# Performance work log

Hardware: AMD Instinct MI355X
Metric: run time of the kernel (lower is better)

The kernel has to match this reference:

```python
import jax, jax.numpy as jnp
import numpy as np

VOCAB, D, H, B, S = 50257, 256, 512, 4096, 256
N_NODES, N_WORLDS = 10, 4
# static in-edge lists derived from SEFIROT_PATHS (to_sefirah == i)
IN_EDGES = [[], [0], [0, 1], [1], [2, 3], [2, 4], [1, 3, 5], [4, 5], [5, 6, 7], [6, 7, 8]]

def _gelu(v):
    return jax.nn.gelu(v, approximate=False)

def setup_inputs() -> dict:
    key = jax.random.key(0)
    ks = jax.random.split(key, 24)
    s = 0.02
    inp = {
        "x": jax.random.randint(ks[0], (B, S), 0, VOCAB, dtype=jnp.int64) if jax.config.jax_enable_x64 else jax.random.randint(ks[0], (B, S), 0, VOCAB, dtype=jnp.int32),
        "num_iterations": 3,
        "embed_table": jax.random.normal(ks[1], (VOCAB, D), jnp.float32) * s,
        # per-node processor MLP (stacked over 10 nodes), weights in [in,out] layout
        "node_w1": jax.random.normal(ks[2], (N_NODES, D, D), jnp.float32) * s,
        "node_b1": jnp.zeros((N_NODES, D), jnp.float32),
        "node_w2": jax.random.normal(ks[3], (N_NODES, D, D), jnp.float32) * s,
        "node_b2": jnp.zeros((N_NODES, D), jnp.float32),
        "recv_w": jax.random.normal(ks[4], (N_NODES, D, D), jnp.float32) * s,
        "recv_b": jnp.zeros((N_NODES, D), jnp.float32),
        # four worlds processors
        "world_w1": jax.random.normal(ks[5], (N_WORLDS, D, D), jnp.float32) * s,
        "world_b1": jnp.zeros((N_WORLDS, D), jnp.float32),
        "world_w2": jax.random.normal(ks[6], (N_WORLDS, D, D), jnp.float32) * s,
        "world_b2": jnp.zeros((N_WORLDS, D), jnp.float32),
        # tzimtzum
        "tz_w1": jax.random.normal(ks[7], (D, D // 2), jnp.float32) * s,
        "tz_b1": jnp.zeros((D // 2,), jnp.float32),
        "tz_w2": jax.random.normal(ks[8], (D // 2, D), jnp.float32) * s,
        "tz_b2": jnp.zeros((D,), jnp.float32),
        "void_space": jax.random.normal(ks[9], (D,), jnp.float32) * 0.1,
        "cre_w": jax.random.normal(ks[10], (D, D), jnp.float32) * s,
        "cre_b": jnp.zeros((D,), jnp.float32),
        # shekhinah head
        "shek_w1": jax.random.normal(ks[11], (D, H), jnp.float32) * s,
        "shek_b1": jnp.zeros((H,), jnp.float32),
        "shek_w2": jax.random.normal(ks[12], (H, 1), jnp.float32) * s,
        "shek_b2": jnp.zeros((1,), jnp.float32),
    }
    return inp

def _forward(embed_table, node_w1, node_b1, node_w2, node_b2, recv_w, recv_b,
             world_w1, world_b1, world_w2, world_b2,
             tz_w1, tz_b1, tz_w2, tz_b2, void_space, cre_w, cre_b,
             shek_w1, shek_b1, shek_w2, shek_b2, x, num_iterations):
    # memory-bound embedding gather [B,S,D] + mean over seq -> [B,D]
    embedded = jnp.take(embed_table, x, axis=0).mean(axis=1)
    states = [embedded] * N_NODES
    # sequential light-flow: node i within an iteration sees updated states of j < i
    for _ in range(int(num_iterations)):
        for i in range(N_NODES):
            h = _gelu(states[i] @ node_w1[i] + node_b1[i]) @ node_w2[i] + node_b2[i]
            srcs = IN_EDGES[i]
            if srcs:
                inc = states[srcs[0]]
                for s_ in srcs[1:]:
                    inc = inc + states[s_]
                h = h + inc @ recv_w[i] + recv_b[i]
            states[i] = h
    malkuth = states[9]
    cur = malkuth
    for w in range(N_WORLDS):
        cur = _gelu(cur @ world_w1[w] + world_b1[w]) @ world_w2[w] + world_b2[w]
    contracted = _gelu(cur @ tz_w1 + tz_b1) @ tz_w2 + tz_b2
    created = (contracted + void_space[None, :]) @ cre_w + cre_b
    shek = jax.nn.sigmoid(_gelu(created @ shek_w1 + shek_b1) @ shek_w2 + shek_b2)  # [B,1]
    # pack all outputs: [B, 10*D + D + D + 1]
    stacked = jnp.concatenate(states, axis=-1)
    return jnp.concatenate([stacked, cur, created, shek], axis=-1)

def reference(x, num_iterations, embed_table, node_w1, node_b1, node_w2, node_b2,
              recv_w, recv_b, world_w1, world_b1, world_w2, world_b2,
              tz_w1, tz_b1, tz_w2, tz_b2, void_space, cre_w, cre_b,
              shek_w1, shek_b1, shek_w2, shek_b2):
    return _forward(embed_table, node_w1, node_b1, node_w2, node_b2, recv_w, recv_b,
                    world_w1, world_b1, world_w2, world_b2,
                    tz_w1, tz_b1, tz_w2, tz_b2, void_space, cre_w, cre_b,
                    shek_w1, shek_b1, shek_w2, shek_b2, x, num_iterations)
```

## Files before the change

kernel.cpp:

```cpp
#include <hip/hip_runtime.h>
#include <hip/hip_bf16.h>

#define DIM 256
#define SEQ 256
#define NB 4096
#define OUT_STRIDE 3073

typedef float f32x4 __attribute__((ext_vector_type(4)));
typedef __bf16 bf16x8 __attribute__((ext_vector_type(8)));
typedef unsigned short u16;
typedef unsigned int u32;

__device__ __forceinline__ float bf2f(u16 h){ return __uint_as_float(((u32)h)<<16); }
__device__ __forceinline__ u16 f2bf(float f){
  u32 u = __float_as_uint(f);
  return (u16)((u + 0x7FFFu + ((u>>16)&1u)) >> 16);
}
__device__ __forceinline__ float gelu_f(float x){
  float u = 0.7978845608028654f*(x + 0.044715f*x*x*x);
  float e = __expf(2.0f*u);
  float t = 1.0f - 2.0f/(e+1.0f);
  return 0.5f*x*(1.0f+t);
}

__device__ const int d_nsrc[10] = {0,1,2,1,2,2,3,2,3,3};
__device__ const int d_srcs[10][3] = {{0,0,0},{0,0,0},{0,1,0},{1,0,0},{2,3,0},
                                      {2,4,0},{1,3,5},{4,5,0},{5,6,7},{6,7,8}};

__global__ void k_convert_table(const float* __restrict__ src, u16* __restrict__ dst, int n4){
  int i = blockIdx.x*blockDim.x + threadIdx.x;
  if (i >= n4) return;
  float4 v = ((const float4*)src)[i];
  ushort4 o; o.x=f2bf(v.x); o.y=f2bf(v.y); o.z=f2bf(v.z); o.w=f2bf(v.w);
  ((ushort4*)dst)[i] = o;
}

__global__ void k_pack(const float* __restrict__ nw1, const float* __restrict__ nw2,
                       const float* __restrict__ rw,  const float* __restrict__ ww1,
                       const float* __restrict__ ww2, const float* __restrict__ tw1,
                       const float* __restrict__ tw2, const float* __restrict__ cw,
                       const float* __restrict__ sw1, u16* __restrict__ dst){
  int g = blockIdx.x*blockDim.x + threadIdx.x;
  if (g >= 344064) return;
  const float* base; int gpm, K, N, segStart;
  if      (g < 81920) { base=nw1; gpm=8192; K=256; N=256; segStart=0; }
  else if (g < 163840){ base=nw2; gpm=8192; K=256; N=256; segStart=81920; }
  else if (g < 245760){ base=rw;  gpm=8192; K=256; N=256; segStart=163840; }
  else if (g < 278528){ base=ww1; gpm=8192; K=256; N=256; segStart=245760; }
  else if (g < 311296){ base=ww2; gpm=8192; K=256; N=256; segStart=278528; }
  else if (g < 315392){ base=tw1; gpm=4096; K=256; N=128; segStart=311296; }
  else if (g < 319488){ base=tw2; gpm=4096; K=128; N=256; segStart=315392; }
  else if (g < 327680){ base=cw;  gpm=8192; K=256; N=256; segStart=319488; }
  else                { base=sw1; gpm=16384;K=256; N=512; segStart=327680; }
  int gs = g - segStart;
  int mat = gs / gpm, gl = gs % gpm;
  int lane = gl & 63, g2 = gl >> 6;
  int Nt = N >> 4;
  int t = g2 % Nt, kk = g2 / Nt;
  int col = t*16 + (lane & 15);
  int k0  = kk*32 + (lane >> 4)*8;
  const float* m = base + (size_t)mat*K*N;
  u16* o = dst + (size_t)g*8;
  (void)K;
  #pragma unroll
  for (int j=0;j<8;j++) o[j] = f2bf(m[(size_t)(k0+j)*N + col]);
}

template<typename T>
__global__ void k_embed(const int* __restrict__ x, const T* __restrict__ table, u16* __restrict__ emb){
  __shared__ float red[4][256];
  int b = blockIdx.x;
  int tid = threadIdx.x, w = tid>>6, lane = tid&63;
  const int* xb = x + b*SEQ;
  float a0=0.f,a1=0.f,a2=0.f,a3=0.f;
  #pragma unroll 4
  for (int ii=0; ii<64; ii++){
    int idx = xb[w*64+ii];
    if constexpr (sizeof(T)==2){
      ushort4 v = *(const ushort4*)(table + (size_t)idx*DIM + lane*4);
      a0+=bf2f(v.x); a1+=bf2f(v.y); a2+=bf2f(v.z); a3+=bf2f(v.w);
    } else {
      float4 v = *(const float4*)(table + (size_t)idx*DIM + lane*4);
      a0+=v.x; a1+=v.y; a2+=v.z; a3+=v.w;
    }
  }
  red[w][lane*4+0]=a0; red[w][lane*4+1]=a1; red[w][lane*4+2]=a2; red[w][lane*4+3]=a3;
  __syncthreads();
  float s = (red[0][tid]+red[1][tid]+red[2][tid]+red[3][tid]) * (1.0f/SEQ);
  emb[(size_t)b*DIM + tid] = f2bf(s);
}

__device__ __forceinline__ bf16x8 lds_readA(const u16* base, int rs, int kk, int lane){
  int row = lane & 15;
  int kbyte = kk*64 + (lane>>4)*16;
  return *(const bf16x8*)((const char*)base + row*rs + (kbyte ^ ((row&7)<<4)));
}

template<int KS>
__device__ __forceinline__ void loadB(bf16x8* dst, const bf16x8* __restrict__ w,
                                      int idx0, int nt, int lane){
  #pragma unroll
  for (int kk=0;kk<KS;kk++) dst[kk] = w[((size_t)(kk*nt+idx0))*64 + lane];
}
template<int KS>
__device__ __forceinline__ void copyB(bf16x8* d, const bf16x8* s){
  #pragma unroll
  for (int kk=0;kk<KS;kk++) d[kk]=s[kk];
}
template<int KS>
__device__ __forceinline__ void mfmaK(const u16* A, int rs, const bf16x8* b, f32x4& acc, int lane){
  #pragma unroll
  for (int kk=0;kk<KS;kk++){
    bf16x8 a = lds_readA(A, rs, kk, lane);
    acc = __builtin_amdgcn_mfma_f32_16x16x32_bf16(a, b[kk], acc, 0, 0, 0);
  }
}

__device__ __forceinline__ f32x4 acc_make(float bv){
  f32x4 t = {bv,bv,bv,bv};
  return t;
}

template<bool GELU>
__device__ __forceinline__ void epi1(f32x4 acc, u16* dst, int rs, int colbase, int lane,
                                     const float* __restrict__ addcol){
  int col = colbase + (lane&15);
  float add = addcol ? addcol[col] : 0.0f;
  #pragma unroll
  for (int r=0;r<4;r++){
    int row = (lane>>4)*4 + r;
    float v = acc[r];
    if (GELU) v = gelu_f(v);
    v += add;
    *(u16*)((char*)dst + row*rs + ((col*2) ^ ((row&7)<<4))) = f2bf(v);
  }
}

__device__ __forceinline__ void out_write(const u16* buf, int rs, float* __restrict__ out,
                                          size_t rowBase, int colBase, int wave, int lane){
  int r = wave;
  int sw = (r&7)<<4;
  #pragma unroll
  for (int cc=0; cc<4; cc++){
    int c = cc*64 + lane;
    float v = bf2f(*(const u16*)((const char*)buf + r*rs + ((c*2)^sw)));
    out[(rowBase + r)*OUT_STRIDE + colBase + c] = v;
  }
}

__global__ __launch_bounds__(1024,4) void k_main(
  const u16* __restrict__ wfrag, const u16* __restrict__ emb,
  const float* __restrict__ nb1, const float* __restrict__ nb2, const float* __restrict__ rb,
  const float* __restrict__ wb1, const float* __restrict__ wb2,
  const float* __restrict__ tb1, const float* __restrict__ tb2,
  const float* __restrict__ voidv, const float* __restrict__ cb,
  const float* __restrict__ sb1, const float* __restrict__ sb2, const float* __restrict__ sw2,
  const int* __restrict__ niter_p, float* __restrict__ out)
{
  __shared__ u16 states[10][16][256];
  __shared__ u16 abuf[16][512];
  __shared__ u16 cbuf[16][256];
  __shared__ u16 hbuf[16][512];
  __shared__ float red[16][65];

  const int tid = threadIdx.x, wave = tid>>6, lane = tid&63;
  const int blk = blockIdx.x;
  const int niter = *niter_p;
  const bf16x8* wf = (const bf16x8*)wfrag;
  const int bcol = wave*16 + (lane&15);

  {
    int r = tid >> 6, c0 = (tid & 63) * 4;
    uint2 v = *(const uint2*)(emb + ((size_t)(blk*16 + r))*DIM + c0);
    int sw = (r&7)<<4;
    #pragma unroll
    for (int st=0; st<10; st++){
      char* bp = (char*)states[st];
      *(uint2*)(bp + r*512 + ((c0*2) ^ sw)) = v;
    }
  }
  __syncthreads();

  bf16x8 bcur[8], bnext[8];
  float bn1, bn2;
  loadB<8>(bcur, (niter>0) ? wf : (wf + 245760), wave, 16, lane);
  bn1 = (niter>0) ? nb1[bcol] : wb1[bcol];
  bn2 = 0.f;

  for (int it=0; it<niter; it++){
    bool last = (it == niter-1);
    for (int i=0; i<10; i++){
      int ns = d_nsrc[i];
      float c1 = bn1;
      loadB<8>(bnext, wf + 81920 + (size_t)i*8192, wave, 16, lane);
      bn1 = nb2[i*DIM + bcol];
      bn2 = (ns>0) ? rb[i*DIM + bcol] : 0.f;
      f32x4 accA = acc_make(c1);
      mfmaK<8>(&states[i][0][0], 512, bcur, accA, lane);
      epi1<true>(accA, &abuf[0][0], 1024, wave*16, lane, nullptr);
      if (ns > 0){
        int r = wave, sw = (r&7)<<4;
        int off = ((lane*8) ^ sw);
        const char* s0 = (const char*)states[d_srcs[i][0]] + r*512;
        const char* s1 = (ns>1) ? ((const char*)states[d_srcs[i][1]] + r*512) : nullptr;
        const char* s2 = (ns>2) ? ((const char*)states[d_srcs[i][2]] + r*512) : nullptr;
        uint2 v0 = *(const uint2*)(s0+off);
        uint2 v1, v2; v1.x=v1.y=0u; v2.x=v2.y=0u;
        if (s1) v1 = *(const uint2*)(s1+off);
        if (s2) v2 = *(const uint2*)(s2+off);
        float ax = __uint_as_float(v0.x<<16) + __uint_as_float(v1.x<<16) + __uint_as_float(v2.x<<16);
        float bx = __uint_as_float(v0.x&0xffff0000u) + __uint_as_float(v1.x&0xffff0000u) + __uint_as_float(v2.x&0xffff0000u);
        float ay = __uint_as_float(v0.y<<16) + __uint_as_float(v1.y<<16) + __uint_as_float(v2.y<<16);
        float by = __uint_as_float(v0.y&0xffff0000u) + __uint_as_float(v1.y&0xffff0000u) + __uint_as_float(v2.y&0xffff0000u);
        uint2 o; o.x = (u32)f2bf(ax) | ((u32)f2bf(bx)<<16);
        o.y = (u32)f2bf(ay) | ((u32)f2bf(by)<<16);
        *(uint2*)((char*)abuf + r*1024 + 512 + off) = o;
      }
      __syncthreads();
      copyB<8>(bcur, bnext);
      float d1 = bn1, d2 = bn2;
      const bf16x8* nextAw = (i<9) ? (wf + (size_t)(i+1)*8192)
                                   : (!last ? wf : (wf + 245760));
      f32x4 accB = acc_make(d1 + d2);
      if (ns > 0){
        loadB<8>(bnext, wf + 163840 + (size_t)i*8192, wave, 16, lane);
        mfmaK<8>(&abuf[0][0], 1024, bcur, accB, lane);
        copyB<8>(bcur, bnext);
        loadB<8>(bnext, nextAw, wave, 16, lane);
        bn1 = (i<9) ? nb1[(i+1)*DIM + bcol] : (!last ? nb1[bcol] : wb1[bcol]);
        bn2 = 0.f;
        mfmaK<8>((const u16*)((const char*)&abuf[0][0] + 512), 1024, bcur, accB, lane);
      } else {
        loadB<8>(bnext, nextAw, wave, 16, lane);
        bn1 = (i<9) ? nb1[(i+1)*DIM + bcol] : (!last ? nb1[bcol] : wb1[bcol]);
        bn2 = 0.f;
        mfmaK<8>(&abuf[0][0], 1024, bcur, accB, lane);
      }
      epi1<false>(accB, &states[i][0][0], 512, wave*16, lane, nullptr);
      __syncthreads();
      copyB<8>(bcur, bnext);
      if (last)
        out_write(&states[i][0][0], 512, out, (size_t)blk*16, i*256, wave, lane);
    }
  }

  for (int w=0; w<4; w++){
    float c1 = bn1;
    loadB<8>(bnext, wf + 278528 + (size_t)w*8192, wave, 16, lane);
    bn1 = wb2[w*DIM + bcol];
    f32x4 a1 = acc_make(c1);
    mfmaK<8>((w==0) ? &states[9][0][0] : &cbuf[0][0], 512, bcur, a1, lane);
    epi1<true>(a1, &abuf[0][0], 1024, wave*16, lane, nullptr);
    __syncthreads();
    copyB<8>(bcur, bnext);
    float d1 = bn1;
    if (w < 3){
      loadB<8>(bnext, wf + 245760 + (size_t)(w+1)*8192, wave, 16, lane);
      bn1 = wb1[(w+1)*DIM + bcol];
    } else {
      loadB<8>(bnext, wf + 311296, wave, 8, lane);
      bn1 = tb1[bcol & 127];
    }
    f32x4 a2 = acc_make(d1);
    mfmaK<8>(&abuf[0][0], 1024, bcur, a2, lane);
    epi1<false>(a2, &cbuf[0][0], 512, wave*16, lane, nullptr);
    __syncthreads();
    copyB<8>(bcur, bnext);
  }
  out_write(&cbuf[0][0], 512, out, (size_t)blk*16, 2560, wave, lane);

  bf16x8 b4[4];
  loadB<4>(b4, wf + 315392, wave, 16, lane);
  {
    float c1 = bn1;
    bn1 = tb2[bcol];
    if (wave < 8){
      f32x4 a = acc_make(c1);
      mfmaK<8>(&cbuf[0][0], 512, bcur, a, lane);
      epi1<true>(a, &abuf[0][0], 1024, wave*16, lane, nullptr);
    }
  }
  __syncthreads();
  loadB<8>(bnext, wf + 319488, wave, 16, lane);
  {
    float c1 = bn1;
    bn1 = cb[bcol];
    f32x4 a = acc_make(c1);
    mfmaK<4>(&abuf[0][0], 1024, b4, a, lane);
    epi1<false>(a, &cbuf[0][0], 512, wave*16, lane, voidv);
  }
  __syncthreads();
  copyB<8>(bcur, bnext);
  loadB<8>(bnext, wf + 327680, wave*2, 32, lane);
  {
    float c1 = bn1;
    bn1 = sb1[wave*32 + (lane&15)];
    bn2 = sb1[wave*32 + 16 + (lane&15)];
    f32x4 a = acc_make(c1);
    mfmaK<8>(&cbuf[0][0], 512, bcur, a, lane);
    epi1<false>(a, &abuf[0][0], 1024, wave*16, lane, nullptr);
  }
  __syncthreads();
  copyB<8>(bcur, bnext);
  loadB<8>(bnext, wf + 327680, wave*2+1, 32, lane);
  {
    f32x4 a0 = acc_make(bn1);
    f32x4 a1 = acc_make(bn2);
    mfmaK<8>(&abuf[0][0], 1024, bcur, a0, lane);
    mfmaK<8>(&abuf[0][0], 1024, bnext, a1, lane);
    epi1<true>(a0, &hbuf[0][0], 1024, (wave*2+0)*16, lane, nullptr);
    epi1<true>(a1, &hbuf[0][0], 1024, (wave*2+1)*16, lane, nullptr);
  }
  __syncthreads();
  {
    int r = tid>>6, p = tid&63;
    int sw = (r&7)<<4;
    float partial = 0.f;
    #pragma unroll
    for (int j=0;j<8;j++){
      int k = p*8+j;
      partial += bf2f(*(const u16*)((const char*)hbuf + r*1024 + ((k*2)^sw))) * sw2[k];
    }
    red[r][p] = partial;
    __syncthreads();
    if (tid < 16){
      float s = sb2[0];
      #pragma unroll
      for (int p2=0;p2<64;p2++) s += red[tid][p2];
      out[((size_t)(blk*16+tid))*OUT_STRIDE + 3072] = 1.f/(1.f+__expf(-s));
    }
  }
  out_write(&abuf[0][0], 1024, out, (size_t)blk*16, 2816, wave, lane);
}

extern "C" void kernel_launch(void* const* d_in, const int* in_sizes, int n_in,
                              void* d_out, int out_size, void* d_ws, size_t ws_size,
                              hipStream_t stream){
  const int*   x     = (const int*)d_in[0];
  const int*   nitp  = (const int*)d_in[1];
  const float* table = (const float*)d_in[2];
  const float* nw1   = (const float*)d_in[3];
  const float* nb1   = (const float*)d_in[4];
  const float* nw2   = (const float*)d_in[5];
  const float* nb2   = (const float*)d_in[6];
  const float* rw    = (const float*)d_in[7];
  const float* rb    = (const float*)d_in[8];
  const float* ww1   = (const float*)d_in[9];
  const float* wb1   = (const float*)d_in[10];
  const float* ww2   = (const float*)d_in[11];
  const float* wb2   = (const float*)d_in[12];
  const float* tw1   = (const float*)d_in[13];
  const float* tb1   = (const float*)d_in[14];
  const float* tw2   = (const float*)d_in[15];
  const float* tb2   = (const float*)d_in[16];
  const float* voidv = (const float*)d_in[17];
  const float* cw    = (const float*)d_in[18];
  const float* cb    = (const float*)d_in[19];
  const float* sw1   = (const float*)d_in[20];
  const float* sb1   = (const float*)d_in[21];
  const float* sw2   = (const float*)d_in[22];
  const float* sb2   = (const float*)d_in[23];
  float* out = (float*)d_out;
  char* ws = (char*)d_ws;

  const size_t TBL_BYTES = (size_t)50257*256*2;
  const size_t WF_BYTES  = (size_t)344064*8*2;
  const size_t EMB_BYTES = (size_t)4096*256*2;
  bool big = ws_size >= TBL_BYTES + WF_BYTES + EMB_BYTES;

  u16 *tbl16, *wfrag, *emb;
  if (big){ tbl16=(u16*)ws; wfrag=(u16*)(ws+TBL_BYTES); emb=(u16*)(ws+TBL_BYTES+WF_BYTES); }
  else    { tbl16=nullptr;  wfrag=(u16*)ws;             emb=(u16*)(ws+WF_BYTES); }

  k_pack<<<1344, 256, 0, stream>>>(nw1,nw2,rw,ww1,ww2,tw1,tw2,cw,sw1,wfrag);
  if (big){
    k_convert_table<<<(3216448+255)/256, 256, 0, stream>>>(table, tbl16, 3216448);
    k_embed<u16><<<NB, 256, 0, stream>>>(x, tbl16, emb);
  } else {
    k_embed<float><<<NB, 256, 0, stream>>>(x, table, emb);
  }
  k_main<<<256, 1024, 0, stream>>>(wfrag, emb, nb1, nb2, rb, wb1, wb2, tb1, tb2,
                                   voidv, cb, sb1, sb2, sw2, nitp, out);
}
```

Before: 343.5 us.

## Use LDS-only barriers and triple weight registers to keep global loads in flight

Replaces __syncthreads with a barrier that waits only on LDS counters (lgkmcnt), so outstanding global weight-fragment loads no longer drain at each barrier. It also restructures the B-fragment buffering into three register sets (b1/b2/b3), so the recv weights and the next layer's weights are fetched earlier, with no copy between buffers. The goal is to overlap weight fetches with MFMA work across barriers. This raises register pressure and relies on the compiler inserting vmcnt waits before each fragment is used.

```diff
diff --git a/kernel.cpp b/kernel.cpp
--- a/kernel.cpp
+++ b/kernel.cpp
@@ -21,6 +21,11 @@
   float e = __expf(2.0f*u);
   float t = 1.0f - 2.0f/(e+1.0f);
   return 0.5f*x*(1.0f+t);
+}
+__device__ __forceinline__ void soft_bar(){
+  asm volatile("s_waitcnt lgkmcnt(0)" ::: "memory");
+  __builtin_amdgcn_s_barrier();
+  asm volatile("" ::: "memory");
 }
 
 __device__ const int d_nsrc[10] = {0,1,2,1,2,2,3,2,3,3};
@@ -103,11 +108,6 @@
   for (int kk=0;kk<KS;kk++) dst[kk] = w[((size_t)(kk*nt+idx0))*64 + lane];
 }
 template<int KS>
-__device__ __forceinline__ void copyB(bf16x8* d, const bf16x8* s){
-  #pragma unroll
-  for (int kk=0;kk<KS;kk++) d[kk]=s[kk];
-}
-template<int KS>
 __device__ __forceinline__ void mfmaK(const u16* A, int rs, const bf16x8* b, f32x4& acc, int lane){
   #pragma unroll
   for (int kk=0;kk<KS;kk++){
@@ -179,24 +179,25 @@
       *(uint2*)(bp + r*512 + ((c0*2) ^ sw)) = v;
     }
   }
-  __syncthreads();
-
-  bf16x8 bcur[8], bnext[8];
+
+  bf16x8 b1[8], b2[8], b3[8];
   float bn1, bn2;
-  loadB<8>(bcur, (niter>0) ? wf : (wf + 245760), wave, 16, lane);
+  loadB<8>(b1, (niter>0) ? wf : (wf + 245760), wave, 16, lane);
   bn1 = (niter>0) ? nb1[bcol] : wb1[bcol];
   bn2 = 0.f;
+  soft_bar();
 
   for (int it=0; it<niter; it++){
     bool last = (it == niter-1);
     for (int i=0; i<10; i++){
       int ns = d_nsrc[i];
+      loadB<8>(b2, wf + 81920 + (size_t)i*8192, wave, 16, lane);
+      if (ns > 0) loadB<8>(b3, wf + 163840 + (size_t)i*8192, wave, 16, lane);
       float c1 = bn1;
-      loadB<8>(bnext, wf + 81920 + (size_t)i*8192, wave, 16, lane);
       bn1 = nb2[i*DIM + bcol];
       bn2 = (ns>0) ? rb[i*DIM + bcol] : 0.f;
       f32x4 accA = acc_make(c1);
-      mfmaK<8>(&states[i][0][0], 512, bcur, accA, lane);
+      mfmaK<8>(&states[i][0][0], 512, b1, accA, lane);
       epi1<true>(accA, &abuf[0][0], 1024, wave*16, lane, nullptr);
       if (ns > 0){
         int r = wave, sw = (r&7)<<4;
@@ -216,102 +217,87 @@
         o.y = (u32)f2bf(ay) | ((u32)f2bf(by)<<16);
         *(uint2*)((char*)abuf + r*1024 + 512 + off) = o;
       }
-      __syncthreads();
-      copyB<8>(bcur, bnext);
+      soft_bar();
       float d1 = bn1, d2 = bn2;
+      f32x4 accB = acc_make(d1 + d2);
+      mfmaK<8>(&abuf[0][0], 1024, b2, accB, lane);
       const bf16x8* nextAw = (i<9) ? (wf + (size_t)(i+1)*8192)
                                    : (!last ? wf : (wf + 245760));
-      f32x4 accB = acc_make(d1 + d2);
-      if (ns > 0){
-        loadB<8>(bnext, wf + 163840 + (size_t)i*8192, wave, 16, lane);
-        mfmaK<8>(&abuf[0][0], 1024, bcur, accB, lane);
-        copyB<8>(bcur, bnext);
-        loadB<8>(bnext, nextAw, wave, 16, lane);
-        bn1 = (i<9) ? nb1[(i+1)*DIM + bcol] : (!last ? nb1[bcol] : wb1[bcol]);
-        bn2 = 0.f;
-        mfmaK<8>((const u16*)((const char*)&abuf[0][0] + 512), 1024, bcur, accB, lane);
-      } else {
-        loadB<8>(bnext, nextAw, wave, 16, lane);
-        bn1 = (i<9) ? nb1[(i+1)*DIM + bcol] : (!last ? nb1[bcol] : wb1[bcol]);
-        bn2 = 0.f;
-        mfmaK<8>(&abuf[0][0], 1024, bcur, accB, lane);
-      }
+      loadB<8>(b1, nextAw, wave, 16, lane);
+      bn1 = (i<9) ? nb1[(i+1)*DIM + bcol] : (!last ? nb1[bcol] : wb1[bcol]);
+      bn2 = 0.f;
+      if (ns > 0)
+        mfmaK<8>((const u16*)((const char*)&abuf[0][0] + 512), 1024, b3, accB, lane);
       epi1<false>(accB, &states[i][0][0], 512, wave*16, lane, nullptr);
-      __syncthreads();
-      copyB<8>(bcur, bnext);
+      soft_bar();
       if (last)
         out_write(&states[i][0][0], 512, out, (size_t)blk*16, i*256, wave, lane);
     }
   }
 
   for (int w=0; w<4; w++){
+    loadB<8>(b2, wf + 278528 + (size_t)w*8192, wave, 16, lane);
     float c1 = bn1;
-    loadB<8>(bnext, wf + 278528 + (size_t)w*8192, wave, 16, lane);
     bn1 = wb2[w*DIM + bcol];
     f32x4 a1 = acc_make(c1);
-    mfmaK<8>((w==0) ? &states[9][0][0] : &cbuf[0][0], 512, bcur, a1, lane);
+    mfmaK<8>((w==0) ? &states[9][0][0] : &cbuf[0][0], 512, b1, a1, lane);
     epi1<true>(a1, &abuf[0][0], 1024, wave*16, lane, nullptr);
-    __syncthreads();
-    copyB<8>(bcur, bnext);
-    float d1 = bn1;
+    soft_bar();
+    f32x4 a2 = acc_make(bn1);
+    mfmaK<8>(&abuf[0][0], 1024, b2, a2, lane);
     if (w < 3){
-      loadB<8>(bnext, wf + 245760 + (size_t)(w+1)*8192, wave, 16, lane);
+      loadB<8>(b1, wf + 245760 + (size_t)(w+1)*8192, wave, 16, lane);
       bn1 = wb1[(w+1)*DIM + bcol];
     } else {
-      loadB<8>(bnext, wf + 311296, wave, 8, lane);
+      loadB<8>(b1, wf + 311296, wave, 8, lane);
       bn1 = tb1[bcol & 127];
     }
-    f32x4 a2 = acc_make(d1);
-    mfmaK<8>(&abuf[0][0], 1024, bcur, a2, lane);
     epi1<false>(a2, &cbuf[0][0], 512, wave*16, lane, nullptr);
-    __syncthreads();
-    copyB<8>(bcur, bnext);
+    soft_bar();
   }
   out_write(&cbuf[0][0], 512, out, (size_t)blk*16, 2560, wave, lane);
 
-  bf16x8 b4[4];
-  loadB<4>(b4, wf + 315392, wave, 16, lane);
+  loadB<4>(b2, wf + 315392, wave, 16, lane);
   {
     float c1 = bn1;
     bn1 = tb2[bcol];
     if (wave < 8){
       f32x4 a = acc_make(c1);
-      mfmaK<8>(&cbuf[0][0], 512, bcur, a, lane);
+      mfmaK<8>(&cbuf[0][0], 512, b1, a, lane);
       epi1<true>(a, &abuf[0][0], 1024, wave*16, lane, nullptr);
     }
   }
-  __syncthreads();
-  loadB<8>(bnext, wf + 319488, wave, 16, lane);
+  soft_bar();
+  loadB<8>(b3, wf + 319488, wave, 16, lane);
   {
     float c1 = bn1;
     bn1 = cb[bcol];
     f32x4 a = acc_make(c1);
-    mfmaK<4>(&abuf[0][0], 1024, b4, a, lane);
+    mfmaK<4>(&abuf[0][0], 1024, b2, a, lane);
     epi1<false>(a, &cbuf[0][0], 512, wave*16, lane, voidv);
   }
-  __syncthreads();
-  copyB<8>(bcur, bnext);
-  loadB<8>(bnext, wf + 327680, wave*2, 32, lane);
+  soft_bar();
+  loadB<8>(b1, wf + 327680, wave*2, 32, lane);
+  loadB<8>(b2, wf + 327680, wave*2+1, 32, lane);
+  float bnS0, bnS1;
   {
     float c1 = bn1;
-    bn1 = sb1[wave*32 + (lane&15)];
-    bn2 = sb1[wave*32 + 16 + (lane&15)];
+    bnS0 = sb1[wave*32 + (lane&15)];
+    bnS1 = sb1[wave*32 + 16 + (lane&15)];
     f32x4 a = acc_make(c1);
-    mfmaK<8>(&cbuf[0][0], 512, bcur, a, lane);
+    mfmaK<8>(&cbuf[0][0], 512, b3, a, lane);
     epi1<false>(a, &abuf[0][0], 1024, wave*16, lane, nullptr);
   }
-  __syncthreads();
-  copyB<8>(bcur, bnext);
-  loadB<8>(bnext, wf + 327680, wave*2+1, 32, lane);
-  {
-    f32x4 a0 = acc_make(bn1);
-    f32x4 a1 = acc_make(bn2);
-    mfmaK<8>(&abuf[0][0], 1024, bcur, a0, lane);
-    mfmaK<8>(&abuf[0][0], 1024, bnext, a1, lane);
+  soft_bar();
+  {
+    f32x4 a0 = acc_make(bnS0);
+    f32x4 a1 = acc_make(bnS1);
+    mfmaK<8>(&abuf[0][0], 1024, b1, a0, lane);
+    mfmaK<8>(&abuf[0][0], 1024, b2, a1, lane);
     epi1<true>(a0, &hbuf[0][0], 1024, (wave*2+0)*16, lane, nullptr);
     epi1<true>(a1, &hbuf[0][0], 1024, (wave*2+1)*16, lane, nullptr);
   }
-  __syncthreads();
+  soft_bar();
   {
     int r = tid>>6, p = tid&63;
     int sw = (r&7)<<4;
@@ -322,7 +308,7 @@
       partial += bf2f(*(const u16*)((const char*)hbuf + r*1024 + ((k*2)^sw))) * sw2[k];
     }
     red[r][p] = partial;
-    __syncthreads();
+    soft_bar();
     if (tid < 16){
       float s = sb2[0];
       #pragma unroll
```

Result: slower. 394.9 us (+15.0%).
